# Optimization experiments

Measured on AMD Instinct MI355X. Metric: run time of the kernel, lower is better.

Reference implementation:

```python
import jax, jax.numpy as jnp
import numpy as np

E = 1024
H = 8
B = 32768
EPS = 1e-5


def setup_inputs() -> dict:
    key = jax.random.key(0)
    ks = jax.random.split(key, 12)
    s = 1.0 / np.sqrt(E)
    return {
        "user_emb": jax.random.normal(ks[0], (B, E), jnp.float32),
        "item_emb": jax.random.normal(ks[1], (B, E), jnp.float32),
        # user_to_item_attention params (torch MultiheadAttention layout)
        "u2i_in_w": jax.random.uniform(ks[2], (3 * E, E), jnp.float32, -s, s),
        "u2i_in_b": jnp.zeros((3 * E,), jnp.float32),
        "u2i_out_w": jax.random.uniform(ks[3], (E, E), jnp.float32, -s, s),
        "u2i_out_b": jnp.zeros((E,), jnp.float32),
        # item_to_user_attention params
        "i2u_in_w": jax.random.uniform(ks[4], (3 * E, E), jnp.float32, -s, s),
        "i2u_in_b": jnp.zeros((3 * E,), jnp.float32),
        "i2u_out_w": jax.random.uniform(ks[5], (E, E), jnp.float32, -s, s),
        "i2u_out_b": jnp.zeros((E,), jnp.float32),
        # LayerNorms
        "user_norm_g": jnp.ones((E,), jnp.float32),
        "user_norm_b": jnp.zeros((E,), jnp.float32),
        "item_norm_g": jnp.ones((E,), jnp.float32),
        "item_norm_b": jnp.zeros((E,), jnp.float32),
        # residual scales
        "alpha": jnp.full((1,), 0.1, jnp.float32),
        "beta": jnp.full((1,), 0.1, jnp.float32),
    }


def _mha_seq1(q_in, kv_in, in_w, in_b, out_w, out_b):
    # torch MHA with query seq_len=1 and key/value seq_len=1 (dropout in eval mode).
    d = E // H
    Wq, Wk, Wv = in_w[:E], in_w[E:2 * E], in_w[2 * E:]
    bq, bk, bv = in_b[:E], in_b[E:2 * E], in_b[2 * E:]
    q = (q_in @ Wq.T + bq).reshape(-1, H, d)   # [B,H,d]
    k = (kv_in @ Wk.T + bk).reshape(-1, H, d)
    v = (kv_in @ Wv.T + bv).reshape(-1, H, d)
    scores = jnp.sum(q * k, axis=-1, keepdims=True) / jnp.sqrt(jnp.float32(d))  # [B,H,1]
    w = jax.nn.softmax(scores, axis=-1)  # single key -> exactly 1
    attn = (w * v).reshape(-1, E)
    return attn @ out_w.T + out_b


def _layernorm(x, g, b):
    mu = jnp.mean(x, axis=-1, keepdims=True)
    var = jnp.mean(jnp.square(x - mu), axis=-1, keepdims=True)
    return (x - mu) * jax.lax.rsqrt(var + EPS) * g + b


def reference(user_emb, item_emb, u2i_in_w, u2i_in_b, u2i_out_w, u2i_out_b,
              i2u_in_w, i2u_in_b, i2u_out_w, i2u_out_b,
              user_norm_g, user_norm_b, item_norm_g, item_norm_b, alpha, beta):
    user_att = _mha_seq1(user_emb, item_emb, u2i_in_w, u2i_in_b, u2i_out_w, u2i_out_b)
    item_att = _mha_seq1(item_emb, user_emb, i2u_in_w, i2u_in_b, i2u_out_w, i2u_out_b)
    user_evolved = _layernorm(user_emb + alpha * user_att, user_norm_g, user_norm_b)
    item_evolved = _layernorm(item_emb + beta * item_att, item_norm_g, item_norm_b)
    return (user_evolved, item_evolved)
```

## Files before the change

kernel.cpp:

```cpp
#include <hip/hip_runtime.h>
#include <cstdint>
#include <cstddef>

#define E 1024
#define NB 32768
#define BM 128
#define BN 128

typedef __attribute__((ext_vector_type(4))) float f32x4;
typedef __attribute__((ext_vector_type(8))) short bf16x8;
typedef __attribute__((ext_vector_type(4))) short s16x4;

__device__ __forceinline__ short f2bfs(float x) {
    __bf16 h = (__bf16)x;
    return __builtin_bit_cast(short, h);
}
__device__ __forceinline__ float bf2f(short u) {
    union { unsigned u; float f; } v;
    v.u = ((unsigned)(unsigned short)u) << 16;
    return v.f;
}
__device__ __forceinline__ bf16x8 cvt8(f32x4 lo, f32x4 hi) {
    bf16x8 r;
#pragma unroll
    for (int j = 0; j < 4; ++j) { r[j] = f2bfs(lo[j]); r[j + 4] = f2bfs(hi[j]); }
    return r;
}

__device__ __forceinline__ void gload16(const void* g, void* l) {
    __builtin_amdgcn_global_load_lds(
        (__attribute__((address_space(1))) void*)g,
        (__attribute__((address_space(3))) void*)l, 16, 0, 0);
}

__global__ __launch_bounds__(256) void wv_transpose(const float* W0, short* T0,
                                                    const float* W1, short* T1) {
    const float* W = blockIdx.z ? W1 : W0;
    short* T = blockIdx.z ? T1 : T0;
    __shared__ float tile[32][33];
    const int j0 = blockIdx.x * 32, i0 = blockIdx.y * 32;
    const int tx = threadIdx.x, ty = threadIdx.y;
#pragma unroll
    for (int r = 0; r < 4; ++r)
        tile[ty + 8 * r][tx] = W[(size_t)(i0 + ty + 8 * r) * E + j0 + tx];
    __syncthreads();
#pragma unroll
    for (int r = 0; r < 4; ++r)
        T[(size_t)(j0 + ty + 8 * r) * E + i0 + tx] = f2bfs(tile[tx][ty + 8 * r]);
}

__global__ __launch_bounds__(256) void bias_fuse(const float* O0, const float* bv0, const float* ob0, const float* s0, float* c0,
                                                 const float* O1, const float* bv1, const float* ob1, const float* s1, float* c1) {
    const float* O  = blockIdx.z ? O1 : O0;
    const float* bv = blockIdx.z ? bv1 : bv0;
    const float* ob = blockIdx.z ? ob1 : ob0;
    const float* sc = blockIdx.z ? s1 : s0;
    float* c = blockIdx.z ? c1 : c0;
    const int n = blockIdx.x, t = threadIdx.x;
    float s = 0.f;
    for (int i = t; i < E; i += 256) s += O[(size_t)n * E + i] * bv[i];
#pragma unroll
    for (int o = 32; o; o >>= 1) s += __shfl_down(s, o);
    __shared__ float rs[4];
    if ((t & 63) == 0) rs[t >> 6] = s;
    __syncthreads();
    if (t == 0) c[n] = sc[0] * (rs[0] + rs[1] + rs[2] + rs[3] + ob[n]);
}

struct GemmArgs {
    const char* A;
    const short* B;
    const float* bias;
    const float* scale;
    char* C;
};

template <bool ABF16>
__global__ __launch_bounds__(256, ABF16 ? 4 : 3) void gemm_bt(GemmArgs g0, GemmArgs g1,
                                                              int mb, int arstride, int crstride) {
    const int nwg = gridDim.x;
    const int q = nwg >> 3;
    const int wgid = (blockIdx.x & 7) * q + (blockIdx.x >> 3);
    const int per = mb * 8;
    const int z = wgid / per;
    const int rem = wgid - z * per;
    const int bx = rem >> 3;
    const int by = rem & 7;
    GemmArgs ga = z ? g1 : g0;

    constexpr int ABYTES = ABF16 ? 8192 : 16384;
    constexpr int BUFB = ABYTES + 8192;
    __shared__ __align__(16) char lds[2][BUFB];

    const int t = threadIdx.x;
    const int l = t & 63, w = t >> 6;
    const int am0 = bx * BM, bn0 = by * BN;

    const char* gA[ABF16 ? 2 : 4];
    if constexpr (ABF16) {
#pragma unroll
        for (int i = 0; i < 2; ++i) {
            int c = i * 4 + w;
            int row = c * 16 + (l >> 2);
            int slot = (l & 3) ^ ((row >> 1) & 3);
            gA[i] = ga.A + (size_t)(am0 + row) * arstride + slot * 16;
        }
    } else {
#pragma unroll
        for (int i = 0; i < 4; ++i) {
            int c = i * 4 + w;
            int row = c * 8 + (l >> 3);
            int slot = (l & 7) ^ (row & 7);
            gA[i] = ga.A + (size_t)(am0 + row) * arstride + slot * 16;
        }
    }
    const short* gB[2];
#pragma unroll
    for (int i = 0; i < 2; ++i) {
        int c = i * 4 + w;
        int row = c * 16 + (l >> 2);
        int slot = (l & 3) ^ ((row >> 1) & 3);
        gB[i] = ga.B + (size_t)(bn0 + row) * E + slot * 8;
    }

    auto stage = [&](int buf, int kt) {
        if constexpr (ABF16) {
#pragma unroll
            for (int i = 0; i < 2; ++i)
                gload16(gA[i] + (size_t)kt * 2, &lds[buf][(i * 4 + w) * 1024]);
        } else {
#pragma unroll
            for (int i = 0; i < 4; ++i)
                gload16(gA[i] + (size_t)kt * 4, &lds[buf][(i * 4 + w) * 1024]);
        }
#pragma unroll
        for (int i = 0; i < 2; ++i)
            gload16(gB[i] + kt, &lds[buf][ABYTES + (i * 4 + w) * 1024]);
    };

    const int wm = w >> 1, wn = w & 1;
    const int r16 = l & 15, kg = l >> 4;
    int aoff[4][ABF16 ? 1 : 2], boff[4];
#pragma unroll
    for (int m = 0; m < 4; ++m) {
        int row = wm * 64 + m * 16 + r16;
        if constexpr (ABF16) {
            aoff[m][0] = row * 64 + (kg ^ ((row >> 1) & 3)) * 16;
        } else {
            aoff[m][0] = row * 128 + ((kg * 2) ^ (row & 7)) * 16;
            aoff[m][1] = row * 128 + ((kg * 2 + 1) ^ (row & 7)) * 16;
        }
    }
#pragma unroll
    for (int n = 0; n < 4; ++n) {
        int row = wn * 64 + n * 16 + r16;
        boff[n] = ABYTES + row * 64 + (kg ^ ((row >> 1) & 3)) * 16;
    }

    f32x4 acc[4][4] = {};

    auto compute = [&](int buf) {
        bf16x8 a[4], b[4];
#pragma unroll
        for (int m = 0; m < 4; ++m) {
            if constexpr (ABF16) {
                a[m] = *(const bf16x8*)&lds[buf][aoff[m][0]];
            } else {
                f32x4 lo = *(const f32x4*)&lds[buf][aoff[m][0]];
                f32x4 hi = *(const f32x4*)&lds[buf][aoff[m][1]];
                a[m] = cvt8(lo, hi);
            }
        }
#pragma unroll
        for (int n = 0; n < 4; ++n)
            b[n] = *(const bf16x8*)&lds[buf][boff[n]];
#pragma unroll
        for (int m = 0; m < 4; ++m)
#pragma unroll
            for (int n = 0; n < 4; ++n)
                acc[m][n] = __builtin_amdgcn_mfma_f32_16x16x32_bf16(a[m], b[n], acc[m][n], 0, 0, 0);
    };

    stage(0, 0);
    __syncthreads();
#pragma unroll 1
    for (int kt = 0; kt < E; kt += 64) {
        stage(1, kt + 32);
        compute(0);
        __syncthreads();
        if (kt + 64 < E) stage(0, kt + 64);
        compute(1);
        __syncthreads();
    }

    const int ccol0 = bn0 + wn * 64 + r16;
    const int crow0 = am0 + wm * 64 + kg * 4;
    const float sc = ga.scale ? ga.scale[0] : 1.f;
    float bn_[4];
#pragma unroll
    for (int n = 0; n < 4; ++n) bn_[n] = ga.bias ? ga.bias[ccol0 + n * 16] : 0.f;
#pragma unroll
    for (int m = 0; m < 4; ++m)
#pragma unroll
        for (int n = 0; n < 4; ++n)
#pragma unroll
            for (int qq = 0; qq < 4; ++qq) {
                int row = crow0 + m * 16 + qq;
                int col = ccol0 + n * 16;
                short* p = (short*)(ga.C + (size_t)row * crstride) + col;
                *p = f2bfs(acc[m][n][qq] * sc + bn_[n]);
            }
}

struct FArgs {
    const float* kv;
    const short* M;
    const float* c;
    const float* q;
    const float* g;
    const float* b;
    float* out;
};

#define B0OFF 8192

__global__ __launch_bounds__(512, 2) void fused_gemm_ln(FArgs f0, FArgs f1) {
    const int bid = blockIdx.x;
    const int u = bid >> 3, xcd = bid & 7;
    const int z = u & 1;
    const int mb = xcd * 64 + (u >> 1);
    const FArgs fa = z ? f1 : f0;
    const int r0 = mb * 64;

    __shared__ __align__(16) char lds[73728];

    const int t = threadIdx.x;
    const int l = t & 63, w = t >> 6;
    const int r16 = l & 15, kg = l >> 4;

    int bsrc[8];
#pragma unroll
    for (int c = 0; c < 8; ++c) {
        int gi = c * 512 + t;
        int row = gi >> 2, slot = gi & 3;
        int ss = slot ^ ((row >> 1) & 3);
        bsrc[c] = row * 2048 + ss * 16;
    }
    const int ar = t >> 3, ach = t & 7;
    const float* asrc = fa.kv + (size_t)(r0 + ar) * E + ach * 4;
    const int awoff = ar * 64 + (((ach >> 1) ^ ((ar >> 1) & 3)) * 16) + (ach & 1) * 8;

    int aoff[4], boff[8];
#pragma unroll
    for (int m = 0; m < 4; ++m) {
        int row = m * 16 + r16;
        aoff[m] = row * 64 + (kg ^ ((row >> 1) & 3)) * 16;
    }
#pragma unroll
    for (int n = 0; n < 8; ++n) {
        int row = w * 128 + n * 16 + r16;
        boff[n] = B0OFF + row * 64 + (kg ^ ((row >> 1) & 3)) * 16;
    }

    f32x4 acc[4][8] = {};

    auto stageB = [&](int kt) {
#pragma unroll
        for (int c = 0; c < 8; ++c)
            gload16((const char*)fa.M + bsrc[c] + kt * 2,
                    &lds[B0OFF + c * 8192 + w * 1024]);
    };
    auto commitA = [&](int buf, f32x4 av) {
        s16x4 v;
#pragma unroll
        for (int j = 0; j < 4; ++j) v[j] = f2bfs(av[j]);
        *(s16x4*)&lds[buf * 4096 + awoff] = v;
    };
    auto compute = [&](int buf) {
        bf16x8 a[4], b[8];
#pragma unroll
        for (int m = 0; m < 4; ++m)
            a[m] = *(const bf16x8*)&lds[buf * 4096 + aoff[m]];
#pragma unroll
        for (int n = 0; n < 8; ++n)
            b[n] = *(const bf16x8*)&lds[boff[n]];
#pragma unroll
        for (int m = 0; m < 4; ++m)
#pragma unroll
            for (int n = 0; n < 8; ++n)
                acc[m][n] = __builtin_amdgcn_mfma_f32_16x16x32_bf16(a[m], b[n], acc[m][n], 0, 0, 0);
    };

    f32x4 a = *(const f32x4*)(asrc);
    stageB(0);
    commitA(0, a);
    a = *(const f32x4*)(asrc + 32);
    __syncthreads();

#pragma unroll 1
    for (int kt = 0; kt < E; kt += 64) {
        compute(0);
        commitA(1, a);
        if (kt + 64 < E) a = *(const f32x4*)(asrc + kt + 64);
        __syncthreads();
        stageB(kt + 32);
        __syncthreads();
        compute(1);
        if (kt + 64 < E) {
            commitA(0, a);
            a = *(const f32x4*)(asrc + kt + 96);
            __syncthreads();
            stageB(kt + 64);
            __syncthreads();
        }
    }
    __syncthreads();

    float* S  = (float*)lds;
    float* Q  = (float*)(lds + 2048);
    float* CB = (float*)(lds + 4096);

    const int colbase = w * 128 + r16;
    float cf[8];
#pragma unroll
    for (int n = 0; n < 8; ++n) cf[n] = fa.c[colbase + n * 16];

    float sum_[4][4] = {}, sq_[4][4] = {};
#pragma unroll
    for (int m = 0; m < 4; ++m) {
#pragma unroll
        for (int n = 0; n < 8; ++n) {
#pragma unroll
            for (int qq = 0; qq < 4; ++qq) {
                int lrow = m * 16 + kg * 4 + qq;
                float x = acc[m][n][qq] + cf[n] + fa.q[(size_t)(r0 + lrow) * E + colbase + n * 16];
                acc[m][n][qq] = x;
                sum_[m][qq] += x;
                sq_[m][qq] += x * x;
            }
        }
    }
#pragma unroll
    for (int m = 0; m < 4; ++m)
#pragma unroll
        for (int qq = 0; qq < 4; ++qq)
#pragma unroll
            for (int o = 1; o < 16; o <<= 1) {
                sum_[m][qq] += __shfl_xor(sum_[m][qq], o);
                sq_[m][qq] += __shfl_xor(sq_[m][qq], o);
            }
#pragma unroll
    for (int m = 0; m < 4; ++m)
#pragma unroll
        for (int qq = 0; qq < 4; ++qq)
            if (r16 == m * 4 + qq) {
                int lrow = m * 16 + kg * 4 + qq;
                S[lrow * 8 + w] = sum_[m][qq];
                Q[lrow * 8 + w] = sq_[m][qq];
            }
    __syncthreads();
    if (t < 64) {
        f32x4 s0 = *(const f32x4*)(S + t * 8);
        f32x4 s1 = *(const f32x4*)(S + t * 8 + 4);
        f32x4 q0 = *(const f32x4*)(Q + t * 8);
        f32x4 q1 = *(const f32x4*)(Q + t * 8 + 4);
        float ss = s0[0] + s0[1] + s0[2] + s0[3] + s1[0] + s1[1] + s1[2] + s1[3];
        float qs = q0[0] + q0[1] + q0[2] + q0[3] + q1[0] + q1[1] + q1[2] + q1[3];
        float mean = ss * (1.0f / E);
        float var = qs * (1.0f / E) - mean * mean;
        CB[t * 2] = mean;
        CB[t * 2 + 1] = rsqrtf(var + 1e-5f);
    }
    __syncthreads();

    float gf[8], bf_[8];
#pragma unroll
    for (int n = 0; n < 8; ++n) {
        gf[n] = fa.g[colbase + n * 16];
        bf_[n] = fa.b[colbase + n * 16];
    }
#pragma unroll
    for (int m = 0; m < 4; ++m)
#pragma unroll
        for (int qq = 0; qq < 4; ++qq) {
            int lrow = m * 16 + kg * 4 + qq;
            float mean = CB[lrow * 2], rstd = CB[lrow * 2 + 1];
            float* op = fa.out + (size_t)(r0 + lrow) * E + colbase;
#pragma unroll
            for (int n = 0; n < 8; ++n)
                op[n * 16] = (acc[m][n][qq] - mean) * rstd * gf[n] + bf_[n];
        }
}

extern "C" void kernel_launch(void* const* d_in, const int* in_sizes, int n_in,
                              void* d_out, int out_size, void* d_ws, size_t ws_size,
                              hipStream_t stream) {
    const float* user_emb = (const float*)d_in[0];
    const float* item_emb = (const float*)d_in[1];
    const float* u2i_in_w = (const float*)d_in[2];
    const float* u2i_in_b = (const float*)d_in[3];
    const float* u2i_out_w = (const float*)d_in[4];
    const float* u2i_out_b = (const float*)d_in[5];
    const float* i2u_in_w = (const float*)d_in[6];
    const float* i2u_in_b = (const float*)d_in[7];
    const float* i2u_out_w = (const float*)d_in[8];
    const float* i2u_out_b = (const float*)d_in[9];
    const float* user_g = (const float*)d_in[10];
    const float* user_b = (const float*)d_in[11];
    const float* item_g = (const float*)d_in[12];
    const float* item_b = (const float*)d_in[13];
    const float* alpha = (const float*)d_in[14];
    const float* beta = (const float*)d_in[15];

    float* out_u = (float*)d_out;
    float* out_i = out_u + (size_t)NB * E;

    short* WvT1 = (short*)d_ws;
    short* WvT2 = WvT1 + (size_t)E * E;
    short* M1 = WvT2 + (size_t)E * E;
    short* M2 = M1 + (size_t)E * E;
    float* c1 = (float*)(M2 + (size_t)E * E);
    float* c2 = c1 + E;

    const dim3 b256(256);

    wv_transpose<<<dim3(32, 32, 2), dim3(32, 8), 0, stream>>>(
        u2i_in_w + 2 * (size_t)E * E, WvT1, i2u_in_w + 2 * (size_t)E * E, WvT2);

    bias_fuse<<<dim3(E, 1, 2), b256, 0, stream>>>(
        u2i_out_w, u2i_in_b + 2 * E, u2i_out_b, alpha, c1,
        i2u_out_w, i2u_in_b + 2 * E, i2u_out_b, beta, c2);

    gemm_bt<false><<<dim3(8 * 8 * 2), b256, 0, stream>>>(
        GemmArgs{(const char*)u2i_out_w, WvT1, nullptr, alpha, (char*)M1},
        GemmArgs{(const char*)i2u_out_w, WvT2, nullptr, beta, (char*)M2},
        8, 4096, 2048);

    fused_gemm_ln<<<dim3(1024), dim3(512), 0, stream>>>(
        FArgs{item_emb, M1, c1, user_emb, user_g, user_b, out_u},
        FArgs{user_emb, M2, c2, item_emb, item_g, item_b, out_i});
}
```

Baseline: 367.2 us.

## Double-buffer A and B tiles via async global-to-LDS loads in fused GEMM

```diff
diff --git a/kernel.cpp b/kernel.cpp
--- a/kernel.cpp
+++ b/kernel.cpp
@@ -222,8 +222,6 @@
     float* out;
 };
 
-#define B0OFF 8192
-
 __global__ __launch_bounds__(512, 2) void fused_gemm_ln(FArgs f0, FArgs f1) {
     const int bid = blockIdx.x;
     const int u = bid >> 3, xcd = bid & 7;
@@ -232,7 +230,7 @@
     const FArgs fa = z ? f1 : f0;
     const int r0 = mb * 64;
 
-    __shared__ __align__(16) char lds[73728];
+    __shared__ __align__(16) char lds[147456];
 
     const int t = threadIdx.x;
     const int l = t & 63, w = t >> 6;
@@ -243,78 +241,82 @@
     for (int c = 0; c < 8; ++c) {
         int gi = c * 512 + t;
         int row = gi >> 2, slot = gi & 3;
-        int ss = slot ^ ((row >> 1) & 3);
-        bsrc[c] = row * 2048 + ss * 16;
-    }
-    const int ar = t >> 3, ach = t & 7;
-    const float* asrc = fa.kv + (size_t)(r0 + ar) * E + ach * 4;
-    const int awoff = ar * 64 + (((ach >> 1) ^ ((ar >> 1) & 3)) * 16) + (ach & 1) * 8;
-
-    int aoff[4], boff[8];
+        bsrc[c] = row * 2048 + (slot ^ ((row >> 1) & 3)) * 16;
+    }
+    const char* Abase = (const char*)fa.kv + (size_t)(r0 + (t >> 3)) * 4096
+                        + ((t & 7) ^ ((t >> 3) & 7)) * 16;
+
+    auto stageB = [&](int buf, int kt) {
+#pragma unroll
+        for (int c = 0; c < 8; ++c)
+            gload16((const char*)fa.M + bsrc[c] + kt * 2,
+                    &lds[16384 + buf * 65536 + c * 8192 + w * 1024]);
+    };
+    auto stageA = [&](int buf, int kt) {
+        gload16(Abase + (size_t)kt * 4, &lds[buf * 8192 + w * 1024]);
+    };
+
+    int aoff0[4], aoff1[4], boff[8];
 #pragma unroll
     for (int m = 0; m < 4; ++m) {
         int row = m * 16 + r16;
-        aoff[m] = row * 64 + (kg ^ ((row >> 1) & 3)) * 16;
+        aoff0[m] = row * 128 + ((kg * 2) ^ (row & 7)) * 16;
+        aoff1[m] = row * 128 + ((kg * 2 + 1) ^ (row & 7)) * 16;
     }
 #pragma unroll
     for (int n = 0; n < 8; ++n) {
         int row = w * 128 + n * 16 + r16;
-        boff[n] = B0OFF + row * 64 + (kg ^ ((row >> 1) & 3)) * 16;
+        boff[n] = 16384 + row * 64 + (kg ^ ((row >> 1) & 3)) * 16;
     }
 
     f32x4 acc[4][8] = {};
 
-    auto stageB = [&](int kt) {
-#pragma unroll
-        for (int c = 0; c < 8; ++c)
-            gload16((const char*)fa.M + bsrc[c] + kt * 2,
-                    &lds[B0OFF + c * 8192 + w * 1024]);
-    };
-    auto commitA = [&](int buf, f32x4 av) {
-        s16x4 v;
-#pragma unroll
-        for (int j = 0; j < 4; ++j) v[j] = f2bfs(av[j]);
-        *(s16x4*)&lds[buf * 4096 + awoff] = v;
-    };
-    auto compute = [&](int buf) {
+    auto phase = [&](int buf, int p) {
+        const int abase = buf * 8192;
+        const int bbase = buf * 65536;
         bf16x8 a[4], b[8];
 #pragma unroll
-        for (int m = 0; m < 4; ++m)
-            a[m] = *(const bf16x8*)&lds[buf * 4096 + aoff[m]];
+        for (int m = 0; m < 4; ++m) {
+            f32x4 lo = *(const f32x4*)&lds[abase + aoff0[m]];
+            f32x4 hi = *(const f32x4*)&lds[abase + aoff1[m]];
+            a[m] = cvt8(lo, hi);
+        }
 #pragma unroll
         for (int n = 0; n < 8; ++n)
-            b[n] = *(const bf16x8*)&lds[boff[n]];
+            b[n] = *(const bf16x8*)&lds[bbase + boff[n]];
+        asm volatile("s_waitcnt lgkmcnt(0)" ::: "memory");
+        __builtin_amdgcn_sched_barrier(0);
+        __builtin_amdgcn_s_barrier();
+        const bool more = (p + 2) < 32;
+        if (more) {
+            stageA(buf, (p + 2) * 32);
+            stageB(buf, (p + 2) * 32);
+        }
+        __builtin_amdgcn_s_setprio(1);
 #pragma unroll
         for (int m = 0; m < 4; ++m)
 #pragma unroll
             for (int n = 0; n < 8; ++n)
                 acc[m][n] = __builtin_amdgcn_mfma_f32_16x16x32_bf16(a[m], b[n], acc[m][n], 0, 0, 0);
+        __builtin_amdgcn_s_setprio(0);
+        if (more) asm volatile("s_waitcnt vmcnt(9)" ::: "memory");
+        else      asm volatile("s_waitcnt vmcnt(0)" ::: "memory");
+        __builtin_amdgcn_sched_barrier(0);
+        __builtin_amdgcn_s_barrier();
     };
 
-    f32x4 a = *(const f32x4*)(asrc);
-    stageB(0);
-    commitA(0, a);
-    a = *(const f32x4*)(asrc + 32);
-    __syncthreads();
+    stageA(0, 0);  stageB(0, 0);
+    stageA(1, 32); stageB(1, 32);
+    asm volatile("s_waitcnt vmcnt(9)" ::: "memory");
+    __builtin_amdgcn_sched_barrier(0);
+    __builtin_amdgcn_s_barrier();
 
 #pragma unroll 1
-    for (int kt = 0; kt < E; kt += 64) {
-        compute(0);
-        commitA(1, a);
-        if (kt + 64 < E) a = *(const f32x4*)(asrc + kt + 64);
-        __syncthreads();
-        stageB(kt + 32);
-        __syncthreads();
-        compute(1);
-        if (kt + 64 < E) {
-            commitA(0, a);
-            a = *(const f32x4*)(asrc + kt + 96);
-            __syncthreads();
-            stageB(kt + 64);
-            __syncthreads();
-        }
-    }
-    __syncthreads();
+    for (int p = 0; p < 32; p += 2) {
+        phase(0, p);
+        phase(1, p + 1);
+    }
+    __builtin_amdgcn_s_barrier();
 
     float* S  = (float*)lds;
     float* Q  = (float*)(lds + 2048);
```

After: 356.2 us. 1.03x faster.
